# Optimization experiments

Measured on AMD Instinct MI355X. Metric: run time of the kernel, lower is better.

The kernel has to match this reference:

```python
import jax, jax.numpy as jnp
import numpy as np

SHAPE = (4096, 8192)


def setup_inputs() -> dict:
    key = jax.random.key(0)
    k1, k2 = jax.random.split(key)
    weights = jax.random.normal(k1, SHAPE, dtype=jnp.float32)
    mask_weights = jax.random.normal(k2, SHAPE, dtype=jnp.float32)
    return {
        "weights": weights,
        "mask_weights": mask_weights,
        "masking_percent_x100": 50,
    }


def reference(weights, mask_weights, masking_percent_x100):
    # Faithful to MaskingFunction.forward:
    #   k = int((1 - masking_percent) * N); zero the k SMALLEST mask_weights positions in weights.
    masking_percent = masking_percent_x100 / 100.0
    n = mask_weights.size  # static
    k = int((1.0 - masking_percent) * n)  # static Python int -> jit-compatible
    flat_mask = mask_weights.reshape(-1)
    # bottom-k == top-k of negated values
    _, bottomk_idx = jax.lax.top_k(-flat_mask, k)
    masked = weights.reshape(-1).at[bottomk_idx].set(0.0)
    return masked.reshape(weights.shape)
```

## Files before the change

### kernel.cpp

```cpp
#include <hip/hip_runtime.h>


#define NBINS 2048
#define CAP1 (1u << 22)
#define CAP2 65536u

__device__ unsigned long long g_k;
__device__ long long          g_b1;
__device__ unsigned long long g_rem1;
__device__ unsigned int       g_hist1[NBINS];
__device__ unsigned int       g_hist2[NBINS];
__device__ unsigned int       g_count1;
__device__ unsigned int       g_count2;
__device__ unsigned long long g_kstar_excl;
__device__ unsigned int       g_cand_u[CAP1];
__device__ unsigned int       g_cand_i[CAP1];
__device__ unsigned long long g_cand2[CAP2];

static __device__ __forceinline__ unsigned int xf(unsigned int b) {
  return b ^ ((unsigned int)((int)b >> 31) | 0x80000000u);
}

__global__ __launch_bounds__(256) void k_init(const int* __restrict__ mp, long long n) {
  int t = threadIdx.x;
  for (int i = t; i < NBINS; i += 256) { g_hist1[i] = 0; g_hist2[i] = 0; }
  if (t == 0) {
    long long m = (long long)(*mp);
    long long k = (n * (100 - m)) / 100;
    if (k < 0) k = 0;
    if (k > n) k = n;
    g_k = (unsigned long long)k;
    g_count1 = 0;
    g_count2 = 0;
    g_kstar_excl = 0;
    g_b1 = -1;
    g_rem1 = 0;
  }
}

__global__ __launch_bounds__(256) void hist1_kernel(const unsigned int* __restrict__ mb,
                                                    long long n4, long long n) {
  __shared__ unsigned int sh[4 * NBINS];
  const int t = threadIdx.x;
  for (int i = t; i < 4 * NBINS; i += 256) sh[i] = 0;
  __syncthreads();
  unsigned int* h = &sh[(t >> 6) * NBINS];
  const long long stride = (long long)gridDim.x * 256;
  const uint4* mb4 = (const uint4*)mb;
  for (long long i = (long long)blockIdx.x * 256 + t; i < n4; i += stride) {
    uint4 v = mb4[i];
    atomicAdd(&h[xf(v.x) >> 21], 1u);
    atomicAdd(&h[xf(v.y) >> 21], 1u);
    atomicAdd(&h[xf(v.z) >> 21], 1u);
    atomicAdd(&h[xf(v.w) >> 21], 1u);
  }
  if (blockIdx.x == 0) {
    long long rs = n4 << 2;
    if ((long long)t < n - rs) atomicAdd(&h[xf(mb[rs + t]) >> 21], 1u);
  }
  __syncthreads();
  for (int i = t; i < NBINS; i += 256) {
    unsigned int s = sh[i] + sh[i + NBINS] + sh[i + 2 * NBINS] + sh[i + 3 * NBINS];
    if (s) atomicAdd(&g_hist1[i], s);
  }
}

__global__ __launch_bounds__(256) void select1_kernel() {
  __shared__ unsigned long long tsum[256];
  __shared__ long long s_bin;
  __shared__ unsigned long long s_rem;
  const int t = threadIdx.x;
  unsigned long long k = g_k;
  if (k == 0) return;
  unsigned int local[8];
  unsigned long long s = 0;
#pragma unroll
  for (int j = 0; j < 8; j++) { local[j] = g_hist1[t * 8 + j]; s += local[j]; }
  tsum[t] = s;
  __syncthreads();
  for (int off = 1; off < 256; off <<= 1) {
    unsigned long long v = (t >= off) ? tsum[t - off] : 0ull;
    __syncthreads();
    tsum[t] += v;
    __syncthreads();
  }
  unsigned long long incl = tsum[t], excl = incl - s;
  if (excl < k && k <= incl) {
    unsigned long long cum = excl;
#pragma unroll
    for (int j = 0; j < 8; j++) {
      if (cum + local[j] >= k) { s_bin = t * 8 + j; s_rem = k - cum; break; }
      cum += local[j];
    }
  }
  __syncthreads();
  if (t == 0) { g_b1 = s_bin; g_rem1 = s_rem; }
}

__global__ __launch_bounds__(256) void pass2_kernel(const unsigned int* __restrict__ mb,
                                                    const float* __restrict__ w,
                                                    float* __restrict__ out,
                                                    long long n4, long long n) {
  __shared__ unsigned int sh2[NBINS];
  const int t = threadIdx.x;
  for (int i = t; i < NBINS; i += 256) sh2[i] = 0;
  __syncthreads();
  const long long b1 = g_b1;
  const long long stride = (long long)gridDim.x * 256;
  const uint4*  mb4 = (const uint4*)mb;
  const float4* w4  = (const float4*)w;
  float4*       o4  = (float4*)out;
  for (long long i = (long long)blockIdx.x * 256 + t; i < n4; i += stride) {
    uint4  mv = mb4[i];
    float4 wv = w4[i];
    unsigned int u0 = xf(mv.x), u1 = xf(mv.y), u2 = xf(mv.z), u3 = xf(mv.w);
    float4 o;
    o.x = ((long long)(u0 >> 21) < b1) ? 0.0f : wv.x;
    o.y = ((long long)(u1 >> 21) < b1) ? 0.0f : wv.y;
    o.z = ((long long)(u2 >> 21) < b1) ? 0.0f : wv.z;
    o.w = ((long long)(u3 >> 21) < b1) ? 0.0f : wv.w;
    o4[i] = o;
    long long base = i << 2;
    if ((long long)(u0 >> 21) == b1) {
      unsigned int s = atomicAdd(&g_count1, 1u);
      if (s < CAP1) { g_cand_u[s] = u0; g_cand_i[s] = (unsigned int)(base + 0); }
      atomicAdd(&sh2[(u0 >> 10) & (NBINS - 1)], 1u);
    }
    if ((long long)(u1 >> 21) == b1) {
      unsigned int s = atomicAdd(&g_count1, 1u);
      if (s < CAP1) { g_cand_u[s] = u1; g_cand_i[s] = (unsigned int)(base + 1); }
      atomicAdd(&sh2[(u1 >> 10) & (NBINS - 1)], 1u);
    }
    if ((long long)(u2 >> 21) == b1) {
      unsigned int s = atomicAdd(&g_count1, 1u);
      if (s < CAP1) { g_cand_u[s] = u2; g_cand_i[s] = (unsigned int)(base + 2); }
      atomicAdd(&sh2[(u2 >> 10) & (NBINS - 1)], 1u);
    }
    if ((long long)(u3 >> 21) == b1) {
      unsigned int s = atomicAdd(&g_count1, 1u);
      if (s < CAP1) { g_cand_u[s] = u3; g_cand_i[s] = (unsigned int)(base + 3); }
      atomicAdd(&sh2[(u3 >> 10) & (NBINS - 1)], 1u);
    }
  }
  if (blockIdx.x == 0) {
    long long rs = n4 << 2;
    long long i = rs + t;
    if (i < n) {
      unsigned int u = xf(mb[i]);
      out[i] = ((long long)(u >> 21) < b1) ? 0.0f : w[i];
      if ((long long)(u >> 21) == b1) {
        unsigned int s = atomicAdd(&g_count1, 1u);
        if (s < CAP1) { g_cand_u[s] = u; g_cand_i[s] = (unsigned int)i; }
        atomicAdd(&sh2[(u >> 10) & (NBINS - 1)], 1u);
      }
    }
  }
  __syncthreads();
  for (int i = t; i < NBINS; i += 256)
    if (sh2[i]) atomicAdd(&g_hist2[i], sh2[i]);
}

__global__ __launch_bounds__(256) void finalize_kernel() {
  __shared__ unsigned long long tsum[256];
  __shared__ long long s_b2;
  __shared__ unsigned long long s_rem2;
  const int t = threadIdx.x;
  long long b1 = g_b1;
  if (b1 < 0) return;
  {
    unsigned long long k = g_rem1;
    unsigned int local[8];
    unsigned long long s = 0;
#pragma unroll
    for (int j = 0; j < 8; j++) { local[j] = g_hist2[t * 8 + j]; s += local[j]; }
    tsum[t] = s;
    __syncthreads();
    for (int off = 1; off < 256; off <<= 1) {
      unsigned long long v = (t >= off) ? tsum[t - off] : 0ull;
      __syncthreads();
      tsum[t] += v;
      __syncthreads();
    }
    unsigned long long incl = tsum[t], excl = incl - s;
    if (excl < k && k <= incl) {
      unsigned long long cum = excl;
#pragma unroll
      for (int j = 0; j < 8; j++) {
        if (cum + local[j] >= k) { s_b2 = t * 8 + j; s_rem2 = k - cum; break; }
        cum += local[j];
      }
    }
    __syncthreads();
  }
  const unsigned int b2 = (unsigned int)s_b2;
  const unsigned int C = (g_count1 < CAP1) ? g_count1 : CAP1;
  for (unsigned int i = t; i < C; i += 256) {
    unsigned int u = g_cand_u[i];
    if (((u >> 10) & (NBINS - 1)) == b2) {
      unsigned int slot = atomicAdd(&g_count2, 1u);
      if (slot < CAP2) g_cand2[slot] = ((unsigned long long)u << 32) | (unsigned long long)g_cand_i[i];
    }
  }
  __threadfence();
  __syncthreads();
  unsigned int c2 = atomicAdd(&g_count2, 0u);
  const unsigned int C2 = (c2 < CAP2) ? c2 : CAP2;
  const unsigned long long rem2 = s_rem2;
  for (unsigned int i = t; i < C2; i += 256) {
    unsigned long long key = g_cand2[i];
    unsigned long long cnt = 0;
    for (unsigned int j = 0; j < C2; j++) cnt += (g_cand2[j] < key) ? 1ull : 0ull;
    if (cnt + 1 == rem2) g_kstar_excl = key + 1;
  }
}

__global__ __launch_bounds__(256) void fixup_kernel(float* __restrict__ out) {
  const unsigned long long kstar = g_kstar_excl;
  const unsigned int C = (g_count1 < CAP1) ? g_count1 : CAP1;
  const long long stride = (long long)gridDim.x * blockDim.x;
  for (long long i = (long long)blockIdx.x * blockDim.x + threadIdx.x; i < (long long)C; i += stride) {
    unsigned int idx = g_cand_i[i];
    unsigned long long key = ((unsigned long long)g_cand_u[i] << 32) | (unsigned long long)idx;
    if (key < kstar) out[idx] = 0.0f;
  }
}

extern "C" void kernel_launch(void* const* d_in, const int* in_sizes, int n_in,
                              void* d_out, int out_size, void* d_ws, size_t ws_size,
                              hipStream_t stream) {
  const float*        w  = (const float*)d_in[0];
  const unsigned int* mb = (const unsigned int*)d_in[1];
  const int*          mp = (const int*)d_in[2];
  float* out = (float*)d_out;
  const long long n  = (long long)in_sizes[0];
  const long long n4 = n >> 2;

  int blocks = (int)((n4 + 255) / 256);
  if (blocks > 2048) blocks = 2048;
  if (blocks < 1) blocks = 1;

  k_init<<<1, 256, 0, stream>>>(mp, n);
  hist1_kernel<<<blocks, 256, 0, stream>>>(mb, n4, n);
  select1_kernel<<<1, 256, 0, stream>>>();
  pass2_kernel<<<blocks, 256, 0, stream>>>(mb, w, out, n4, n);
  finalize_kernel<<<1, 256, 0, stream>>>();
  fixup_kernel<<<256, 256, 0, stream>>>(out);
}
```

Baseline: 366.9 us.

## Restructure radix select into three kernels with byte histograms and warp-aggregated capture

The select pipeline goes from six kernels to three. The first pass now builds a 256-bin histogram on the top 8 bits, using per-thread byte counters in shared memory instead of shared atomics. The bin selection is folded into the second pass, which now captures candidates with wavefront-aggregated atomics. The single-block finalize kernel builds the second histogram, does the rank selection in shared memory, applies the fixup and resets global state for the next call. The cost is a much larger first-level candidate set (about 1/256 of the elements instead of about 1/2048), all processed by one block. Byte counters can also overflow when a thread sees more than 255 hits in one bin: with 8192 uint4 per block, each thread handles about 32 values, so this is safe only for inputs of this size.

Result: slower. 462.5 us (+26.1%).

```diff
diff --git a/kernel.cpp b/kernel.cpp
--- a/kernel.cpp
+++ b/kernel.cpp
@@ -1,248 +1,250 @@
 #include <hip/hip_runtime.h>
 
 
-#define NBINS 2048
-#define CAP1 (1u << 22)
-#define CAP2 65536u
-
-__device__ unsigned long long g_k;
-__device__ long long          g_b1;
-__device__ unsigned long long g_rem1;
-__device__ unsigned int       g_hist1[NBINS];
-__device__ unsigned int       g_hist2[NBINS];
-__device__ unsigned int       g_count1;
-__device__ unsigned int       g_count2;
-__device__ unsigned long long g_kstar_excl;
-__device__ unsigned int       g_cand_u[CAP1];
-__device__ unsigned int       g_cand_i[CAP1];
-__device__ unsigned long long g_cand2[CAP2];
-
-static __device__ __forceinline__ unsigned int xf(unsigned int b) {
-  return b ^ ((unsigned int)((int)b >> 31) | 0x80000000u);
-}
-
-__global__ __launch_bounds__(256) void k_init(const int* __restrict__ mp, long long n) {
-  int t = threadIdx.x;
-  for (int i = t; i < NBINS; i += 256) { g_hist1[i] = 0; g_hist2[i] = 0; }
-  if (t == 0) {
-    long long m = (long long)(*mp);
-    long long k = (n * (100 - m)) / 100;
-    if (k < 0) k = 0;
-    if (k > n) k = n;
-    g_k = (unsigned long long)k;
-    g_count1 = 0;
-    g_count2 = 0;
-    g_kstar_excl = 0;
-    g_b1 = -1;
-    g_rem1 = 0;
-  }
-}
-
-__global__ __launch_bounds__(256) void hist1_kernel(const unsigned int* __restrict__ mb,
+typedef unsigned int u32;
+typedef unsigned long long u64;
+
+#define NB1 256
+#define NB2 2048
+#define CAP1 (1u << 20)
+#define CAP2 2048u
+
+__device__ u32 g_hist1[NB1];
+__device__ u32 g_count1;
+__device__ u32 g_cand_u[CAP1];
+__device__ u32 g_cand_i[CAP1];
+
+static __device__ __forceinline__ u32 xf(u32 b) {
+  return b ^ ((u32)((int)b >> 31) | 0x80000000u);
+}
+static __device__ __forceinline__ u32 sb(u32 v) {
+  return (v & 0xFFu) + ((v >> 8) & 0xFFu) + ((v >> 16) & 0xFFu) + (v >> 24);
+}
+static __device__ __forceinline__ long long calc_k(int mpv, long long n) {
+  long long k = (n * (long long)(100 - mpv)) / 100;
+  if (k < 0) k = 0;
+  if (k > n) k = n;
+  return k;
+}
+
+static __device__ __forceinline__ void capture(u32 u, u32 idx, bool pred, int lane) {
+  u64 m = __ballot(pred);
+  if (m == 0ull) return;
+  int lead = __ffsll((unsigned long long)m) - 1;
+  u32 base = 0;
+  if (lane == lead) base = atomicAdd(&g_count1, (u32)__popcll(m));
+  base = __shfl(base, lead);
+  if (pred) {
+    u32 pos = base + (u32)__popcll(m & ((1ull << lane) - 1ull));
+    if (pos < CAP1) { g_cand_u[pos] = u; g_cand_i[pos] = idx; }
+  }
+}
+
+__global__ __launch_bounds__(256) void hist1_kernel(const u32* __restrict__ mb,
                                                     long long n4, long long n) {
-  __shared__ unsigned int sh[4 * NBINS];
+  __shared__ unsigned char sh[NB1 * 256];
   const int t = threadIdx.x;
-  for (int i = t; i < 4 * NBINS; i += 256) sh[i] = 0;
-  __syncthreads();
-  unsigned int* h = &sh[(t >> 6) * NBINS];
+  {
+    uint4* s4 = (uint4*)sh;
+#pragma unroll
+    for (int i = 0; i < 16; i++) s4[i * 256 + t] = make_uint4(0u, 0u, 0u, 0u);
+  }
+  __syncthreads();
+  unsigned char* base = sh + ((t & 63) << 2) + (t >> 6);
   const long long stride = (long long)gridDim.x * 256;
   const uint4* mb4 = (const uint4*)mb;
   for (long long i = (long long)blockIdx.x * 256 + t; i < n4; i += stride) {
     uint4 v = mb4[i];
-    atomicAdd(&h[xf(v.x) >> 21], 1u);
-    atomicAdd(&h[xf(v.y) >> 21], 1u);
-    atomicAdd(&h[xf(v.z) >> 21], 1u);
-    atomicAdd(&h[xf(v.w) >> 21], 1u);
+    base[(xf(v.x) >> 24) << 8] += 1;
+    base[(xf(v.y) >> 24) << 8] += 1;
+    base[(xf(v.z) >> 24) << 8] += 1;
+    base[(xf(v.w) >> 24) << 8] += 1;
   }
   if (blockIdx.x == 0) {
     long long rs = n4 << 2;
-    if ((long long)t < n - rs) atomicAdd(&h[xf(mb[rs + t]) >> 21], 1u);
-  }
-  __syncthreads();
-  for (int i = t; i < NBINS; i += 256) {
-    unsigned int s = sh[i] + sh[i + NBINS] + sh[i + 2 * NBINS] + sh[i + 3 * NBINS];
-    if (s) atomicAdd(&g_hist1[i], s);
-  }
-}
-
-__global__ __launch_bounds__(256) void select1_kernel() {
-  __shared__ unsigned long long tsum[256];
-  __shared__ long long s_bin;
-  __shared__ unsigned long long s_rem;
-  const int t = threadIdx.x;
-  unsigned long long k = g_k;
-  if (k == 0) return;
-  unsigned int local[8];
-  unsigned long long s = 0;
-#pragma unroll
-  for (int j = 0; j < 8; j++) { local[j] = g_hist1[t * 8 + j]; s += local[j]; }
-  tsum[t] = s;
-  __syncthreads();
-  for (int off = 1; off < 256; off <<= 1) {
-    unsigned long long v = (t >= off) ? tsum[t - off] : 0ull;
-    __syncthreads();
-    tsum[t] += v;
-    __syncthreads();
-  }
-  unsigned long long incl = tsum[t], excl = incl - s;
-  if (excl < k && k <= incl) {
-    unsigned long long cum = excl;
-#pragma unroll
-    for (int j = 0; j < 8; j++) {
-      if (cum + local[j] >= k) { s_bin = t * 8 + j; s_rem = k - cum; break; }
-      cum += local[j];
-    }
-  }
-  __syncthreads();
-  if (t == 0) { g_b1 = s_bin; g_rem1 = s_rem; }
-}
-
-__global__ __launch_bounds__(256) void pass2_kernel(const unsigned int* __restrict__ mb,
+    if ((long long)t < n - rs) base[(xf(mb[rs + t]) >> 24) << 8] += 1;
+  }
+  __syncthreads();
+  const uint4* row = (const uint4*)(sh + (t << 8));
+  u32 s = 0;
+#pragma unroll
+  for (int j = 0; j < 16; j++) {
+    uint4 v = row[(j + t) & 15];
+    s += sb(v.x) + sb(v.y) + sb(v.z) + sb(v.w);
+  }
+  if (s) atomicAdd(&g_hist1[t], s);
+}
+
+__global__ __launch_bounds__(256) void pass2_kernel(const u32* __restrict__ mb,
                                                     const float* __restrict__ w,
                                                     float* __restrict__ out,
+                                                    const int* __restrict__ mp,
                                                     long long n4, long long n) {
-  __shared__ unsigned int sh2[NBINS];
+  __shared__ u32 scan[256];
+  __shared__ int s_b1;
   const int t = threadIdx.x;
-  for (int i = t; i < NBINS; i += 256) sh2[i] = 0;
-  __syncthreads();
-  const long long b1 = g_b1;
+  if (t == 0) s_b1 = -1;
+  const long long k = calc_k(*mp, n);
+  u32 c = g_hist1[t];
+  u32 x = c;
+  scan[t] = x;
+  __syncthreads();
+  for (int off = 1; off < 256; off <<= 1) {
+    u32 v = (t >= off) ? scan[t - off] : 0u;
+    __syncthreads();
+    x += v;
+    scan[t] = x;
+    __syncthreads();
+  }
+  if (k > 0 && (long long)(x - c) < k && k <= (long long)x) s_b1 = t;
+  __syncthreads();
+  const int b1 = s_b1;
+  const int lane = t & 63;
   const long long stride = (long long)gridDim.x * 256;
-  const uint4*  mb4 = (const uint4*)mb;
-  const float4* w4  = (const float4*)w;
-  float4*       o4  = (float4*)out;
+  const uint4* mb4 = (const uint4*)mb;
+  const float4* w4 = (const float4*)w;
+  float4* o4 = (float4*)out;
   for (long long i = (long long)blockIdx.x * 256 + t; i < n4; i += stride) {
-    uint4  mv = mb4[i];
+    uint4 mv = mb4[i];
     float4 wv = w4[i];
-    unsigned int u0 = xf(mv.x), u1 = xf(mv.y), u2 = xf(mv.z), u3 = xf(mv.w);
+    u32 u0 = xf(mv.x), u1 = xf(mv.y), u2 = xf(mv.z), u3 = xf(mv.w);
+    int c0 = (int)(u0 >> 24), c1 = (int)(u1 >> 24), c2 = (int)(u2 >> 24), c3 = (int)(u3 >> 24);
     float4 o;
-    o.x = ((long long)(u0 >> 21) < b1) ? 0.0f : wv.x;
-    o.y = ((long long)(u1 >> 21) < b1) ? 0.0f : wv.y;
-    o.z = ((long long)(u2 >> 21) < b1) ? 0.0f : wv.z;
-    o.w = ((long long)(u3 >> 21) < b1) ? 0.0f : wv.w;
+    o.x = (c0 < b1) ? 0.0f : wv.x;
+    o.y = (c1 < b1) ? 0.0f : wv.y;
+    o.z = (c2 < b1) ? 0.0f : wv.z;
+    o.w = (c3 < b1) ? 0.0f : wv.w;
     o4[i] = o;
-    long long base = i << 2;
-    if ((long long)(u0 >> 21) == b1) {
-      unsigned int s = atomicAdd(&g_count1, 1u);
-      if (s < CAP1) { g_cand_u[s] = u0; g_cand_i[s] = (unsigned int)(base + 0); }
-      atomicAdd(&sh2[(u0 >> 10) & (NBINS - 1)], 1u);
-    }
-    if ((long long)(u1 >> 21) == b1) {
-      unsigned int s = atomicAdd(&g_count1, 1u);
-      if (s < CAP1) { g_cand_u[s] = u1; g_cand_i[s] = (unsigned int)(base + 1); }
-      atomicAdd(&sh2[(u1 >> 10) & (NBINS - 1)], 1u);
-    }
-    if ((long long)(u2 >> 21) == b1) {
-      unsigned int s = atomicAdd(&g_count1, 1u);
-      if (s < CAP1) { g_cand_u[s] = u2; g_cand_i[s] = (unsigned int)(base + 2); }
-      atomicAdd(&sh2[(u2 >> 10) & (NBINS - 1)], 1u);
-    }
-    if ((long long)(u3 >> 21) == b1) {
-      unsigned int s = atomicAdd(&g_count1, 1u);
-      if (s < CAP1) { g_cand_u[s] = u3; g_cand_i[s] = (unsigned int)(base + 3); }
-      atomicAdd(&sh2[(u3 >> 10) & (NBINS - 1)], 1u);
-    }
+    u32 bidx = (u32)(i << 2);
+    capture(u0, bidx + 0u, c0 == b1, lane);
+    capture(u1, bidx + 1u, c1 == b1, lane);
+    capture(u2, bidx + 2u, c2 == b1, lane);
+    capture(u3, bidx + 3u, c3 == b1, lane);
   }
   if (blockIdx.x == 0) {
     long long rs = n4 << 2;
     long long i = rs + t;
-    if (i < n) {
-      unsigned int u = xf(mb[i]);
-      out[i] = ((long long)(u >> 21) < b1) ? 0.0f : w[i];
-      if ((long long)(u >> 21) == b1) {
-        unsigned int s = atomicAdd(&g_count1, 1u);
-        if (s < CAP1) { g_cand_u[s] = u; g_cand_i[s] = (unsigned int)i; }
-        atomicAdd(&sh2[(u >> 10) & (NBINS - 1)], 1u);
+    bool act = i < n;
+    u32 u = 0;
+    bool pred = false;
+    if (act) {
+      u = xf(mb[i]);
+      int b = (int)(u >> 24);
+      out[i] = (b < b1) ? 0.0f : w[i];
+      pred = (b == b1);
+    }
+    capture(u, (u32)i, pred, lane);
+  }
+}
+
+__global__ __launch_bounds__(256) void finalize_kernel(const int* __restrict__ mp,
+                                                       long long n,
+                                                       float* __restrict__ out) {
+  __shared__ u32 h2[NB2];
+  __shared__ u64 k2[CAP2];
+  __shared__ u32 scan[256];
+  __shared__ int s_b1, s_b2;
+  __shared__ u32 s_rem1, s_rem2, s_c2;
+  __shared__ u64 s_kstar;
+  const int t = threadIdx.x;
+  if (t == 0) { s_b1 = -1; s_b2 = 0; s_rem1 = 0; s_rem2 = 0; s_c2 = 0; s_kstar = 0ull; }
+  const long long k = calc_k(*mp, n);
+  u32 c = g_hist1[t];
+  u32 x = c;
+  scan[t] = x;
+  __syncthreads();
+  for (int off = 1; off < 256; off <<= 1) {
+    u32 v = (t >= off) ? scan[t - off] : 0u;
+    __syncthreads();
+    x += v;
+    scan[t] = x;
+    __syncthreads();
+  }
+  if (k > 0 && (long long)(x - c) < k && k <= (long long)x) {
+    s_b1 = t;
+    s_rem1 = (u32)(k - (long long)(x - c));
+  }
+  __syncthreads();
+  const int b1 = s_b1;
+  if (b1 >= 0) {
+    const u32 C = min(g_count1, CAP1);
+    for (int i = t; i < NB2; i += 256) h2[i] = 0u;
+    __syncthreads();
+    for (u32 i = (u32)t; i < C; i += 256) atomicAdd(&h2[(g_cand_u[i] >> 13) & (NB2 - 1u)], 1u);
+    __syncthreads();
+    u32 loc[8];
+    u32 s = 0;
+#pragma unroll
+    for (int j = 0; j < 8; j++) { loc[j] = h2[t * 8 + j]; s += loc[j]; }
+    u32 y = s;
+    scan[t] = y;
+    __syncthreads();
+    for (int off = 1; off < 256; off <<= 1) {
+      u32 v = (t >= off) ? scan[t - off] : 0u;
+      __syncthreads();
+      y += v;
+      scan[t] = y;
+      __syncthreads();
+    }
+    const u32 rem1 = s_rem1;
+    u32 excl2 = y - s;
+    if (excl2 < rem1 && rem1 <= y) {
+      u32 cum = excl2;
+#pragma unroll
+      for (int j = 0; j < 8; j++) {
+        if (cum + loc[j] >= rem1) { s_b2 = t * 8 + j; s_rem2 = rem1 - cum; break; }
+        cum += loc[j];
       }
     }
-  }
-  __syncthreads();
-  for (int i = t; i < NBINS; i += 256)
-    if (sh2[i]) atomicAdd(&g_hist2[i], sh2[i]);
-}
-
-__global__ __launch_bounds__(256) void finalize_kernel() {
-  __shared__ unsigned long long tsum[256];
-  __shared__ long long s_b2;
-  __shared__ unsigned long long s_rem2;
-  const int t = threadIdx.x;
-  long long b1 = g_b1;
-  if (b1 < 0) return;
-  {
-    unsigned long long k = g_rem1;
-    unsigned int local[8];
-    unsigned long long s = 0;
-#pragma unroll
-    for (int j = 0; j < 8; j++) { local[j] = g_hist2[t * 8 + j]; s += local[j]; }
-    tsum[t] = s;
-    __syncthreads();
-    for (int off = 1; off < 256; off <<= 1) {
-      unsigned long long v = (t >= off) ? tsum[t - off] : 0ull;
-      __syncthreads();
-      tsum[t] += v;
-      __syncthreads();
-    }
-    unsigned long long incl = tsum[t], excl = incl - s;
-    if (excl < k && k <= incl) {
-      unsigned long long cum = excl;
-#pragma unroll
-      for (int j = 0; j < 8; j++) {
-        if (cum + local[j] >= k) { s_b2 = t * 8 + j; s_rem2 = k - cum; break; }
-        cum += local[j];
+    __syncthreads();
+    const u32 b2 = (u32)s_b2;
+    for (u32 i = (u32)t; i < C; i += 256) {
+      u32 u = g_cand_u[i];
+      if (((u >> 13) & (NB2 - 1u)) == b2) {
+        u32 slot = atomicAdd(&s_c2, 1u);
+        if (slot < CAP2) k2[slot] = ((u64)u << 32) | (u64)g_cand_i[i];
       }
     }
     __syncthreads();
-  }
-  const unsigned int b2 = (unsigned int)s_b2;
-  const unsigned int C = (g_count1 < CAP1) ? g_count1 : CAP1;
-  for (unsigned int i = t; i < C; i += 256) {
-    unsigned int u = g_cand_u[i];
-    if (((u >> 10) & (NBINS - 1)) == b2) {
-      unsigned int slot = atomicAdd(&g_count2, 1u);
-      if (slot < CAP2) g_cand2[slot] = ((unsigned long long)u << 32) | (unsigned long long)g_cand_i[i];
-    }
-  }
-  __threadfence();
-  __syncthreads();
-  unsigned int c2 = atomicAdd(&g_count2, 0u);
-  const unsigned int C2 = (c2 < CAP2) ? c2 : CAP2;
-  const unsigned long long rem2 = s_rem2;
-  for (unsigned int i = t; i < C2; i += 256) {
-    unsigned long long key = g_cand2[i];
-    unsigned long long cnt = 0;
-    for (unsigned int j = 0; j < C2; j++) cnt += (g_cand2[j] < key) ? 1ull : 0ull;
-    if (cnt + 1 == rem2) g_kstar_excl = key + 1;
-  }
-}
-
-__global__ __launch_bounds__(256) void fixup_kernel(float* __restrict__ out) {
-  const unsigned long long kstar = g_kstar_excl;
-  const unsigned int C = (g_count1 < CAP1) ? g_count1 : CAP1;
-  const long long stride = (long long)gridDim.x * blockDim.x;
-  for (long long i = (long long)blockIdx.x * blockDim.x + threadIdx.x; i < (long long)C; i += stride) {
-    unsigned int idx = g_cand_i[i];
-    unsigned long long key = ((unsigned long long)g_cand_u[i] << 32) | (unsigned long long)idx;
-    if (key < kstar) out[idx] = 0.0f;
-  }
+    const u32 C2 = min(s_c2, CAP2);
+    const u32 rem2 = s_rem2;
+    for (u32 i = (u32)t; i < C2; i += 256) {
+      u64 key = k2[i];
+      u32 cnt = 0;
+      for (u32 j = 0; j < C2; j++) cnt += (k2[j] < key) ? 1u : 0u;
+      if (cnt + 1u == rem2) s_kstar = key + 1ull;
+    }
+    __syncthreads();
+    const u64 kstar = s_kstar;
+    for (u32 i = (u32)t; i < C; i += 256) {
+      u32 idx = g_cand_i[i];
+      u64 key = ((u64)g_cand_u[i] << 32) | (u64)idx;
+      if (key < kstar) out[idx] = 0.0f;
+    }
+  }
+  __syncthreads();
+  g_hist1[t] = 0u;
+  if (t == 0) g_count1 = 0u;
 }
 
 extern "C" void kernel_launch(void* const* d_in, const int* in_sizes, int n_in,
                               void* d_out, int out_size, void* d_ws, size_t ws_size,
                               hipStream_t stream) {
-  const float*        w  = (const float*)d_in[0];
-  const unsigned int* mb = (const unsigned int*)d_in[1];
-  const int*          mp = (const int*)d_in[2];
+  const float* w  = (const float*)d_in[0];
+  const u32*   mb = (const u32*)d_in[1];
+  const int*   mp = (const int*)d_in[2];
   float* out = (float*)d_out;
   const long long n  = (long long)in_sizes[0];
   const long long n4 = n >> 2;
 
-  int blocks = (int)((n4 + 255) / 256);
-  if (blocks > 2048) blocks = 2048;
-  if (blocks < 1) blocks = 1;
-
-  k_init<<<1, 256, 0, stream>>>(mp, n);
-  hist1_kernel<<<blocks, 256, 0, stream>>>(mb, n4, n);
-  select1_kernel<<<1, 256, 0, stream>>>();
-  pass2_kernel<<<blocks, 256, 0, stream>>>(mb, w, out, n4, n);
-  finalize_kernel<<<1, 256, 0, stream>>>();
-  fixup_kernel<<<256, 256, 0, stream>>>(out);
-}
+  long long hb = (n4 + 8191) / 8192;
+  if (hb < 1) hb = 1;
+  if (hb > 16384) hb = 16384;
+  long long pb = (n4 + 255) / 256;
+  if (pb < 1) pb = 1;
+  if (pb > 4096) pb = 4096;
+
+  hist1_kernel<<<(int)hb, 256, 0, stream>>>(mb, n4, n);
+  pass2_kernel<<<(int)pb, 256, 0, stream>>>(mb, w, out, mp, n4, n);
+  finalize_kernel<<<1, 256, 0, stream>>>(mp, n, out);
+}
```
